# Kernel optimization log

Measured on AMD Instinct MI355X. Metric: run time of the kernel, lower is better.

The kernel has to match this reference:

```python
import jax, jax.numpy as jnp
import numpy as np

N_NODES = 50000
N_EDGES = 1600000
HIDDEN = 128
N_RBF = 50


def _linear_init(key, fan_in, fan_out):
    # mimic torch nn.Linear default init: U(-1/sqrt(fan_in), 1/sqrt(fan_in))
    kw, kb = jax.random.split(key)
    bound = 1.0 / np.sqrt(fan_in)
    W = jax.random.uniform(kw, (fan_in, fan_out), minval=-bound, maxval=bound, dtype=jnp.float32)
    b = jax.random.uniform(kb, (fan_out,), minval=-bound, maxval=bound, dtype=jnp.float32)
    return W, b


def setup_inputs() -> dict:
    key = jax.random.key(0)
    ks = jax.random.split(key, 9)
    x = jax.random.normal(ks[0], (N_NODES, HIDDEN), dtype=jnp.float32)
    edge_index = jax.random.randint(ks[1], (2, N_EDGES), 0, N_NODES, dtype=jnp.int32)
    edge_attr = jax.random.uniform(ks[2], (N_EDGES, N_RBF), dtype=jnp.float32)
    fW1, fb1 = _linear_init(ks[3], N_RBF, HIDDEN)
    fW2, fb2 = _linear_init(ks[4], HIDDEN, HIDDEN)
    dW, db = _linear_init(ks[5], HIDDEN, HIDDEN)
    uW1, ub1 = _linear_init(ks[6], HIDDEN, HIDDEN)
    uW2, ub2 = _linear_init(ks[7], HIDDEN, HIDDEN)
    return {
        "x": x, "edge_index": edge_index, "edge_attr": edge_attr,
        "fW1": fW1, "fb1": fb1, "fW2": fW2, "fb2": fb2,
        "dW": dW, "db": db,
        "uW1": uW1, "ub1": ub1, "uW2": uW2, "ub2": ub2,
    }


def reference(x, edge_index, edge_attr, fW1, fb1, fW2, fb2, dW, db, uW1, ub1, uW2, ub2):
    src, dst = edge_index[0], edge_index[1]
    # filter network: Linear -> SiLU -> Linear on edge RBF features [E, n_rbf] -> [E, H]
    filters = jax.nn.silu(edge_attr @ fW1 + fb1) @ fW2 + fb2
    # messages: dense(x[src]) * filters  [E, H]
    messages = (x[src] @ dW + db) * filters
    # scatter-add to destination nodes
    aggregated = jax.ops.segment_sum(messages, dst, num_segments=x.shape[0])
    # update MLP + residual
    upd = jax.nn.silu(aggregated @ uW1 + ub1) @ uW2 + ub2
    return x + upd
```

## Files before the change

### kernel.cpp

```cpp
#include <hip/hip_runtime.h>

#define H    128
#define RBF  50
#define K1   64
#define EB   64
#define NB   32
#define NBLK 1024

typedef _Float16 f16;
typedef _Float16 f16x4 __attribute__((ext_vector_type(4)));
typedef _Float16 f16x8 __attribute__((ext_vector_type(8)));
typedef float    f32x4 __attribute__((ext_vector_type(4)));

#define HS_LD 136

__device__ __forceinline__ float silu_f(float a) {
    return a / (1.0f + __expf(-a));
}


__global__ __launch_bounds__(256) void hist_kernel(
    const int* __restrict__ dst, int* __restrict__ counts, int E)
{
    for (int i = blockIdx.x * 256 + threadIdx.x; i < E; i += gridDim.x * 256)
        atomicAdd(&counts[dst[i]], 1);
}

__global__ __launch_bounds__(256) void scan1_kernel(
    const int* __restrict__ counts, int* __restrict__ ofs, int* __restrict__ bsum, int N)
{
    __shared__ int s[256];
    const int t = threadIdx.x;
    const int g = blockIdx.x * 256 + t;
    int v = (g < N) ? counts[g] : 0;
    s[t] = v; __syncthreads();
    for (int off = 1; off < 256; off <<= 1) {
        int u = 0; if (t >= off) u = s[t - off];
        __syncthreads(); s[t] += u; __syncthreads();
    }
    if (g < N) ofs[g] = s[t] - v;
    if (t == 255) bsum[blockIdx.x] = s[255];
}
__global__ __launch_bounds__(256) void scan2_kernel(int* __restrict__ bsum, int nb)
{
    __shared__ int s[256];
    const int t = threadIdx.x;
    int v = (t < nb) ? bsum[t] : 0;
    s[t] = v; __syncthreads();
    for (int off = 1; off < 256; off <<= 1) {
        int u = 0; if (t >= off) u = s[t - off];
        __syncthreads(); s[t] += u; __syncthreads();
    }
    if (t < nb) bsum[t] = s[t] - v;
}
__global__ __launch_bounds__(256) void scan3_kernel(
    int* __restrict__ ofs, int* __restrict__ cursor, const int* __restrict__ bsum, int N)
{
    int g = blockIdx.x * 256 + threadIdx.x;
    if (g < N) {
        int v = ofs[g] + bsum[blockIdx.x];
        ofs[g] = v;
        cursor[g] = v;
    }
}

__global__ __launch_bounds__(256) void ranges_kernel(
    const int* __restrict__ ofs, int* __restrict__ nstart, int* __restrict__ estart,
    int N, int E, int B)
{
    int b = blockIdx.x * 256 + threadIdx.x;
    if (b > B) return;
    if (b == B) { nstart[B] = N; estart[B] = E; return; }
    long long cb = (long long)b * E / B;
    int lo = 0, hi = N;
    while (lo < hi) {
        int mid = (lo + hi) >> 1;
        int val = (mid < N) ? ofs[mid] : E;
        if (val < (int)cb) lo = mid + 1; else hi = mid;
    }
    nstart[b] = lo;
    estart[b] = (lo < N) ? ofs[lo] : E;
}

__global__ __launch_bounds__(256) void scatter_kernel(
    const int* __restrict__ src, const int* __restrict__ dst,
    int* __restrict__ cursor, int* __restrict__ rank, int2* __restrict__ sd, int E)
{
    for (int i = blockIdx.x * 256 + threadIdx.x; i < E; i += gridDim.x * 256) {
        int d = dst[i];
        int pos = atomicAdd(&cursor[d], 1);
        rank[i] = pos;
        sd[pos] = make_int2(src[i], d);
    }
}

__global__ __launch_bounds__(256) void permute_ea_kernel(
    const float* __restrict__ ea, const int* __restrict__ rank,
    f16* __restrict__ ea16, int E)
{
    const int tid = threadIdx.x;
    const int e = blockIdx.x * EB + (tid >> 2);
    const int s = tid & 3;
    if (e >= E) return;
    const int p = rank[e];
    const float* rp = ea + (size_t)e * RBF;

    const float4 a = *(const float4*)(rp + s * 8);
    const float4 b = *(const float4*)(rp + s * 8 + 4);
    float4 c4 = {}, d4 = {};
    if (s < 2) {
        c4 = *(const float4*)(rp + 32 + s * 8);
        d4 = *(const float4*)(rp + 36 + s * 8);
    } else if (s == 2) {
        const float2 t2 = *(const float2*)(rp + 48);
        c4.x = t2.x; c4.y = t2.y;
    }
    f16x8 v1, v2;
    v1[0]=(f16)a.x; v1[1]=(f16)a.y; v1[2]=(f16)a.z; v1[3]=(f16)a.w;
    v1[4]=(f16)b.x; v1[5]=(f16)b.y; v1[6]=(f16)b.z; v1[7]=(f16)b.w;
    v2[0]=(f16)c4.x; v2[1]=(f16)c4.y; v2[2]=(f16)c4.z; v2[3]=(f16)c4.w;
    v2[4]=(f16)d4.x; v2[5]=(f16)d4.y; v2[6]=(f16)d4.z; v2[7]=(f16)d4.w;

    f16* op = ea16 + (size_t)p * K1;
    *(f16x8*)(op + s * 8)      = v1;
    *(f16x8*)(op + 32 + s * 8) = v2;
}


__global__ __launch_bounds__(256) void convert_weights_kernel(
    const float* __restrict__ fW1, const float* __restrict__ fW2,
    f16* __restrict__ Wt1, f16* __restrict__ Wt2)
{
    int i = blockIdx.x * 256 + threadIdx.x;
    if (i < H * K1) {
        int n = i >> 6, k = i & (K1 - 1);
        Wt1[i] = (k < RBF) ? (f16)fW1[k * H + n] : (f16)0.f;
    }
    int j = i - H * K1;
    if (j >= 0 && j < H * H) {
        int n = j >> 7, k = j & (H - 1);
        Wt2[j] = (f16)fW2[k * H + n];
    }
}

__global__ __launch_bounds__(256) void compute_h_kernel(
    const float* __restrict__ x, const float* __restrict__ dW,
    const float* __restrict__ db, f16* __restrict__ h, int N)
{
    __shared__ float xs[NB][H];
    const int tid = threadIdx.x;
    const int n0  = blockIdx.x * NB;
    for (int idx = tid; idx < NB * H; idx += 256) {
        int r = idx >> 7, c = idx & (H - 1);
        int n = n0 + r;
        xs[r][c] = (n < N) ? x[(size_t)n * H + c] : 0.f;
    }
    __syncthreads();
    const int j  = tid & (H - 1);
    const int rb = (tid >> 7) * 16;
    float acc[16];
    const float b = db[j];
#pragma unroll
    for (int r = 0; r < 16; ++r) acc[r] = b;
    for (int kq = 0; kq < H / 4; ++kq) {
        const int k = kq * 4;
        const float w0 = dW[(k + 0) * H + j];
        const float w1 = dW[(k + 1) * H + j];
        const float w2 = dW[(k + 2) * H + j];
        const float w3 = dW[(k + 3) * H + j];
#pragma unroll
        for (int r = 0; r < 16; ++r) {
            const float4 v = *(const float4*)&xs[rb + r][k];
            acc[r] = fmaf(v.x, w0, fmaf(v.y, w1, fmaf(v.z, w2, fmaf(v.w, w3, acc[r]))));
        }
    }
#pragma unroll
    for (int r = 0; r < 16; ++r) {
        int n = n0 + rb + r;
        if (n < N) h[(size_t)n * H + j] = (f16)acc[r];
    }
}

__global__ __launch_bounds__(256, 4) void edge_fused_kernel(
    const f16* __restrict__ ea16, const int2* __restrict__ sd,
    const f16* __restrict__ Wt1, const f16* __restrict__ Wt2,
    const float* __restrict__ fb1, const float* __restrict__ fb2,
    const f16* __restrict__ h, float* __restrict__ out,
    const int* __restrict__ nstart, const int* __restrict__ estart, int E)
{
    __shared__ __align__(16) f16 uni[8192];
    __shared__ __align__(16) f16 h_s[EB * HS_LD];
    __shared__ int dst_s[EB];

    const int tid  = threadIdx.x;
    const int lane = tid & 63;
    const int wv   = tid >> 6;
    const int wr   = (wv >> 1) * 32;
    const int wc   = (wv & 1) * 64;
    const int fr   = lane & 15;
    const int qw   = lane >> 4;
    const int kb   = qw * 8;

    const int j = tid >> 2;
    const int s = tid & 3;

    f16x8 B1[4][2];
    f16x8 B2[4][4];
    float b1v[4], b2v[4];
#pragma unroll
    for (int ct = 0; ct < 4; ++ct) {
        const int col = wc + ct * 16 + fr;
#pragma unroll
        for (int ks = 0; ks < 2; ++ks)
            B1[ct][ks] = *(const f16x8*)&Wt1[col * K1 + ks * 32 + kb];
#pragma unroll
        for (int ks = 0; ks < 4; ++ks)
            B2[ct][ks] = *(const f16x8*)&Wt2[col * H + ks * 32 + kb];
        b1v[ct] = fb1[col];
        b2v[ct] = fb2[col];
    }

    const int ns = nstart[blockIdx.x], ne = nstart[blockIdx.x + 1];
    const int e0 = estart[blockIdx.x], e1 = estart[blockIdx.x + 1];

    if (e0 >= e1) {
        for (int idx = tid; idx < (ne - ns) * H; idx += 256)
            out[(size_t)ns * H + idx] = 0.f;
        return;
    }

    const int col128 = tid & 127;
    int   curdst = ns;
    float accv   = 0.f;

    int2 sdP;
    { int idx = e0 + j; idx = (idx < e1) ? idx : (e1 - 1); sdP = sd[idx]; }

    for (int tb = e0; tb < e1; tb += EB) {
        int2 sdN;
        { int idx = tb + EB + j; idx = (idx < e1) ? idx : (e1 - 1); sdN = sd[idx]; }

        {
            const f16* hp = h + (size_t)sdP.x * H + s * 8;
            const f16x8 h0 = *(const f16x8*)(hp);
            const f16x8 h1 = *(const f16x8*)(hp + 32);
            const f16x8 h2 = *(const f16x8*)(hp + 64);
            const f16x8 h3 = *(const f16x8*)(hp + 96);

            const int pe = tb + j;
            const f16* ep = ea16 + (size_t)((pe < E) ? pe : (E - 1)) * K1;
            const f16x8 ev1 = *(const f16x8*)(ep + s * 8);
            const f16x8 ev2 = *(const f16x8*)(ep + 32 + s * 8);

            *(f16x8*)&h_s[j * HS_LD +  0 + s * 8] = h0;
            *(f16x8*)&h_s[j * HS_LD + 32 + s * 8] = h1;
            *(f16x8*)&h_s[j * HS_LD + 64 + s * 8] = h2;
            *(f16x8*)&h_s[j * HS_LD + 96 + s * 8] = h3;
            *(f16x8*)((char*)uni + (size_t)(((s)     * 64 + j) * 16)) = ev1;
            *(f16x8*)((char*)uni + (size_t)(((4 + s) * 64 + j) * 16)) = ev2;
            if (s == 0) dst_s[j] = (pe < e1) ? sdP.y : ne;
        }
        __syncthreads();

        f32x4 acc1[2][4];
#pragma unroll
        for (int rt = 0; rt < 2; ++rt)
#pragma unroll
            for (int ct = 0; ct < 4; ++ct)
                acc1[rt][ct] = (f32x4){b1v[ct], b1v[ct], b1v[ct], b1v[ct]};
#pragma unroll
        for (int ks = 0; ks < 2; ++ks) {
            const f16x8 A0 = *(const f16x8*)((char*)uni + (size_t)(((ks * 4 + qw) * 64 + wr + fr) * 16));
            const f16x8 A1 = *(const f16x8*)((char*)uni + (size_t)(((ks * 4 + qw) * 64 + wr + 16 + fr) * 16));
#pragma unroll
            for (int ct = 0; ct < 4; ++ct) {
                acc1[0][ct] = __builtin_amdgcn_mfma_f32_16x16x32_f16(A0, B1[ct][ks], acc1[0][ct], 0, 0, 0);
                acc1[1][ct] = __builtin_amdgcn_mfma_f32_16x16x32_f16(A1, B1[ct][ks], acc1[1][ct], 0, 0, 0);
            }
        }
        __syncthreads();

#pragma unroll
        for (int rt = 0; rt < 2; ++rt)
#pragma unroll
            for (int ct = 0; ct < 4; ++ct)
#pragma unroll
                for (int m = 0; m < 4; ++m) {
                    const int er = wr + rt * 16 + qw * 4 + m;
                    const int c  = wc + ct * 16 + fr;
                    *(f16*)((char*)uni + (size_t)(((c >> 3) * 64 + er) * 16 + (c & 7) * 2)) =
                        (f16)silu_f(acc1[rt][ct][m]);
                }
        __syncthreads();

        f32x4 acc2[2][4];
#pragma unroll
        for (int rt = 0; rt < 2; ++rt)
#pragma unroll
            for (int ct = 0; ct < 4; ++ct)
                acc2[rt][ct] = (f32x4){b2v[ct], b2v[ct], b2v[ct], b2v[ct]};
#pragma unroll
        for (int ks = 0; ks < 4; ++ks) {
            const f16x8 A0 = *(const f16x8*)((char*)uni + (size_t)(((ks * 4 + qw) * 64 + wr + fr) * 16));
            const f16x8 A1 = *(const f16x8*)((char*)uni + (size_t)(((ks * 4 + qw) * 64 + wr + 16 + fr) * 16));
#pragma unroll
            for (int ct = 0; ct < 4; ++ct) {
                acc2[0][ct] = __builtin_amdgcn_mfma_f32_16x16x32_f16(A0, B2[ct][ks], acc2[0][ct], 0, 0, 0);
                acc2[1][ct] = __builtin_amdgcn_mfma_f32_16x16x32_f16(A1, B2[ct][ks], acc2[1][ct], 0, 0, 0);
            }
        }

#pragma unroll
        for (int rt = 0; rt < 2; ++rt)
#pragma unroll
            for (int ct = 0; ct < 4; ++ct)
#pragma unroll
                for (int m = 0; m < 4; ++m) {
                    const int er = wr + rt * 16 + qw * 4 + m;
                    const int c  = wc + ct * 16 + fr;
                    f16* p = &h_s[er * HS_LD + c];
                    *p = (f16)((float)*p * acc2[rt][ct][m]);
                }
        __syncthreads();

        if (tid < 128) {
            for (int r = 0; r < EB; ++r) {
                const int d = dst_s[r];
                const float v = (float)h_s[r * HS_LD + col128];
                if (d != curdst) {
                    out[(size_t)curdst * H + col128] = accv;
                    for (int n = curdst + 1; n < d; ++n) out[(size_t)n * H + col128] = 0.f;
                    curdst = d; accv = 0.f;
                }
                if (d < ne) accv += v;
            }
        }
        __syncthreads();

        sdP = sdN;
    }

    if (tid < 128 && curdst < ne) {
        out[(size_t)curdst * H + col128] = accv;
        for (int n = curdst + 1; n < ne; ++n) out[(size_t)n * H + col128] = 0.f;
    }
}

__global__ __launch_bounds__(256) void update_kernel(
    const float* __restrict__ x,
    const float* __restrict__ uW1, const float* __restrict__ ub1,
    const float* __restrict__ uW2, const float* __restrict__ ub2,
    float* __restrict__ out, int N)
{
    __shared__ float as[NB][H];
    __shared__ float ts[NB][H];
    const int tid = threadIdx.x;
    const int n0  = blockIdx.x * NB;
    for (int idx = tid; idx < NB * H; idx += 256) {
        int r = idx >> 7, c = idx & (H - 1);
        int n = n0 + r;
        as[r][c] = (n < N) ? out[(size_t)n * H + c] : 0.f;
    }
    __syncthreads();
    const int j  = tid & (H - 1);
    const int rb = (tid >> 7) * 16;
    float acc[16];
    {
        const float b1 = ub1[j];
#pragma unroll
        for (int r = 0; r < 16; ++r) acc[r] = b1;
    }
    for (int kq = 0; kq < H / 4; ++kq) {
        const int k = kq * 4;
        const float w0 = uW1[(k + 0) * H + j];
        const float w1 = uW1[(k + 1) * H + j];
        const float w2 = uW1[(k + 2) * H + j];
        const float w3 = uW1[(k + 3) * H + j];
#pragma unroll
        for (int r = 0; r < 16; ++r) {
            const float4 v = *(const float4*)&as[rb + r][k];
            acc[r] = fmaf(v.x, w0, fmaf(v.y, w1, fmaf(v.z, w2, fmaf(v.w, w3, acc[r]))));
        }
    }
#pragma unroll
    for (int r = 0; r < 16; ++r) ts[rb + r][j] = silu_f(acc[r]);
    __syncthreads();
    {
        const float b2 = ub2[j];
#pragma unroll
        for (int r = 0; r < 16; ++r) acc[r] = b2;
    }
    for (int kq = 0; kq < H / 4; ++kq) {
        const int k = kq * 4;
        const float w0 = uW2[(k + 0) * H + j];
        const float w1 = uW2[(k + 1) * H + j];
        const float w2 = uW2[(k + 2) * H + j];
        const float w3 = uW2[(k + 3) * H + j];
#pragma unroll
        for (int r = 0; r < 16; ++r) {
            const float4 v = *(const float4*)&ts[rb + r][k];
            acc[r] = fmaf(v.x, w0, fmaf(v.y, w1, fmaf(v.z, w2, fmaf(v.w, w3, acc[r]))));
        }
    }
#pragma unroll
    for (int r = 0; r < 16; ++r) {
        int n = n0 + rb + r;
        if (n < N) out[(size_t)n * H + j] = x[(size_t)n * H + j] + acc[r];
    }
}

extern "C" void kernel_launch(void* const* d_in, const int* in_sizes, int n_in,
                              void* d_out, int out_size, void* d_ws, size_t ws_size,
                              hipStream_t stream) {
    const float* x   = (const float*)d_in[0];
    const int*   ei  = (const int*)  d_in[1];
    const float* ea  = (const float*)d_in[2];
    const float* fW1 = (const float*)d_in[3];
    const float* fb1 = (const float*)d_in[4];
    const float* fW2 = (const float*)d_in[5];
    const float* fb2 = (const float*)d_in[6];
    const float* dW  = (const float*)d_in[7];
    const float* db  = (const float*)d_in[8];
    const float* uW1 = (const float*)d_in[9];
    const float* ub1 = (const float*)d_in[10];
    const float* uW2 = (const float*)d_in[11];
    const float* ub2 = (const float*)d_in[12];

    float* out = (float*)d_out;
    const int N = in_sizes[0] / H;
    const int E = in_sizes[1] / 2;
    const int* src = ei;
    const int* dst = ei + E;

    char* ws = (char*)d_ws;
    size_t off = 0;
    auto alloc = [&](size_t bytes) { void* p = ws + off; off = (off + bytes + 255) & ~(size_t)255; return p; };
    f16*  h      = (f16*) alloc((size_t)N * H * sizeof(f16));
    f16*  Wt1    = (f16*) alloc((size_t)H * K1 * sizeof(f16));
    f16*  Wt2    = (f16*) alloc((size_t)H * H * sizeof(f16));
    int*  counts = (int*) alloc((size_t)N * sizeof(int));
    int*  ofs    = (int*) alloc((size_t)N * sizeof(int));
    int*  cursor = (int*) alloc((size_t)N * sizeof(int));
    int*  bsum   = (int*) alloc(256 * sizeof(int));
    int*  nstart = (int*) alloc((size_t)(NBLK + 1) * sizeof(int));
    int*  estart = (int*) alloc((size_t)(NBLK + 1) * sizeof(int));
    int*  rank   = (int*) alloc((size_t)E * sizeof(int));
    int2* sd     = (int2*)alloc((size_t)E * sizeof(int2));
    f16*  ea16   = (f16*) alloc((size_t)E * K1 * sizeof(f16));

    const int nscan  = (N + 255) / 256;
    const int ntiles = (E + EB - 1) / EB;

    hipMemsetAsync(counts, 0, (size_t)N * sizeof(int), stream);
    convert_weights_kernel<<<(H * K1 + H * H + 255) / 256, 256, 0, stream>>>(fW1, fW2, Wt1, Wt2);
    compute_h_kernel<<<(N + NB - 1) / NB, 256, 0, stream>>>(x, dW, db, h, N);

    hist_kernel<<<2048, 256, 0, stream>>>(dst, counts, E);
    scan1_kernel<<<nscan, 256, 0, stream>>>(counts, ofs, bsum, N);
    scan2_kernel<<<1, 256, 0, stream>>>(bsum, nscan);
    scan3_kernel<<<nscan, 256, 0, stream>>>(ofs, cursor, bsum, N);

    ranges_kernel<<<(NBLK + 256) / 256, 256, 0, stream>>>(ofs, nstart, estart, N, E, NBLK);
    scatter_kernel<<<2048, 256, 0, stream>>>(src, dst, cursor, rank, sd, E);
    permute_ea_kernel<<<ntiles, 256, 0, stream>>>(ea, rank, ea16, E);

    edge_fused_kernel<<<NBLK, 256, 0, stream>>>(
        ea16, sd, Wt1, Wt2, fb1, fb2, h, out, nstart, estart, E);

    update_kernel<<<(N + NB - 1) / NB, 256, 0, stream>>>(
        x, uW1, ub1, uW2, ub2, out, N);
}
```

Before: 947.3 us.

## Fuse prep kernels, merge scatter with edge-attr permute, double-buffer src/dst in LDS

Merges the weight conversion, node dense projection and destination histogram into one launch split by block index. Fuses the scatter and fp16 edge-attribute permutation into one pass, which drops the rank array and its extra read/write. In the edge kernel, src/dst indices are now staged through double-buffered shared memory, loaded by otherwise idle threads during the reduction phase, and gathered h rows are copied with a different lane mapping. The new build kernel has each thread write a full 128-byte row with weaker coalescing on the uncoalesced ea reads, which may offset the saved pass.

```diff
diff --git a/kernel.cpp b/kernel.cpp
--- a/kernel.cpp
+++ b/kernel.cpp
@@ -19,12 +19,67 @@
 }
 
 
-__global__ __launch_bounds__(256) void hist_kernel(
+__global__ __launch_bounds__(256) void prep1_kernel(
+    const float* __restrict__ x, const float* __restrict__ dW,
+    const float* __restrict__ db, f16* __restrict__ h, int N, int nH,
+    const float* __restrict__ fW1, const float* __restrict__ fW2,
+    f16* __restrict__ Wt1, f16* __restrict__ Wt2,
     const int* __restrict__ dst, int* __restrict__ counts, int E)
 {
-    for (int i = blockIdx.x * 256 + threadIdx.x; i < E; i += gridDim.x * 256)
-        atomicAdd(&counts[dst[i]], 1);
-}
+    __shared__ float xs[NB][H];
+    const int tid = threadIdx.x;
+    const int b   = blockIdx.x;
+
+    if (b < nH) {
+        const int n0 = b * NB;
+        for (int idx = tid; idx < NB * H; idx += 256) {
+            int r = idx >> 7, c = idx & (H - 1);
+            int n = n0 + r;
+            xs[r][c] = (n < N) ? x[(size_t)n * H + c] : 0.f;
+        }
+        __syncthreads();
+        const int j  = tid & (H - 1);
+        const int rb = (tid >> 7) * 16;
+        float acc[16];
+        const float bb = db[j];
+#pragma unroll
+        for (int r = 0; r < 16; ++r) acc[r] = bb;
+        for (int kq = 0; kq < H / 4; ++kq) {
+            const int k = kq * 4;
+            const float w0 = dW[(k + 0) * H + j];
+            const float w1 = dW[(k + 1) * H + j];
+            const float w2 = dW[(k + 2) * H + j];
+            const float w3 = dW[(k + 3) * H + j];
+#pragma unroll
+            for (int r = 0; r < 16; ++r) {
+                const float4 v = *(const float4*)&xs[rb + r][k];
+                acc[r] = fmaf(v.x, w0, fmaf(v.y, w1, fmaf(v.z, w2, fmaf(v.w, w3, acc[r]))));
+            }
+        }
+#pragma unroll
+        for (int r = 0; r < 16; ++r) {
+            int n = n0 + rb + r;
+            if (n < N) h[(size_t)n * H + j] = (f16)acc[r];
+        }
+    } else if (b < nH + 96) {
+        int i = (b - nH) * 256 + tid;
+        if (i < H * K1) {
+            int n = i >> 6, k = i & (K1 - 1);
+            Wt1[i] = (k < RBF) ? (f16)fW1[k * H + n] : (f16)0.f;
+        }
+        int jj = i - H * K1;
+        if (jj >= 0 && jj < H * H) {
+            int n = jj >> 7, k = jj & (H - 1);
+            Wt2[jj] = (f16)fW2[k * H + n];
+        }
+    } else {
+        const int hb  = b - nH - 96;
+        const int hgd = gridDim.x - nH - 96;
+        for (int i = hb * 256 + tid; i < E; i += hgd * 256)
+            atomicAdd(&counts[dst[i]], 1);
+    }
+}
+
 
 __global__ __launch_bounds__(256) void scan1_kernel(
     const int* __restrict__ counts, int* __restrict__ ofs, int* __restrict__ bsum, int N)
@@ -82,102 +137,36 @@
     estart[b] = (lo < N) ? ofs[lo] : E;
 }
 
-__global__ __launch_bounds__(256) void scatter_kernel(
-    const int* __restrict__ src, const int* __restrict__ dst,
-    int* __restrict__ cursor, int* __restrict__ rank, int2* __restrict__ sd, int E)
-{
-    for (int i = blockIdx.x * 256 + threadIdx.x; i < E; i += gridDim.x * 256) {
-        int d = dst[i];
-        int pos = atomicAdd(&cursor[d], 1);
-        rank[i] = pos;
-        sd[pos] = make_int2(src[i], d);
-    }
-}
-
-__global__ __launch_bounds__(256) void permute_ea_kernel(
-    const float* __restrict__ ea, const int* __restrict__ rank,
-    f16* __restrict__ ea16, int E)
-{
-    const int tid = threadIdx.x;
-    const int e = blockIdx.x * EB + (tid >> 2);
-    const int s = tid & 3;
-    if (e >= E) return;
-    const int p = rank[e];
-    const float* rp = ea + (size_t)e * RBF;
-
-    const float4 a = *(const float4*)(rp + s * 8);
-    const float4 b = *(const float4*)(rp + s * 8 + 4);
-    float4 c4 = {}, d4 = {};
-    if (s < 2) {
-        c4 = *(const float4*)(rp + 32 + s * 8);
-        d4 = *(const float4*)(rp + 36 + s * 8);
-    } else if (s == 2) {
-        const float2 t2 = *(const float2*)(rp + 48);
-        c4.x = t2.x; c4.y = t2.y;
-    }
-    f16x8 v1, v2;
-    v1[0]=(f16)a.x; v1[1]=(f16)a.y; v1[2]=(f16)a.z; v1[3]=(f16)a.w;
-    v1[4]=(f16)b.x; v1[5]=(f16)b.y; v1[6]=(f16)b.z; v1[7]=(f16)b.w;
-    v2[0]=(f16)c4.x; v2[1]=(f16)c4.y; v2[2]=(f16)c4.z; v2[3]=(f16)c4.w;
-    v2[4]=(f16)d4.x; v2[5]=(f16)d4.y; v2[6]=(f16)d4.z; v2[7]=(f16)d4.w;
-
-    f16* op = ea16 + (size_t)p * K1;
-    *(f16x8*)(op + s * 8)      = v1;
-    *(f16x8*)(op + 32 + s * 8) = v2;
-}
-
-
-__global__ __launch_bounds__(256) void convert_weights_kernel(
-    const float* __restrict__ fW1, const float* __restrict__ fW2,
-    f16* __restrict__ Wt1, f16* __restrict__ Wt2)
-{
-    int i = blockIdx.x * 256 + threadIdx.x;
-    if (i < H * K1) {
-        int n = i >> 6, k = i & (K1 - 1);
-        Wt1[i] = (k < RBF) ? (f16)fW1[k * H + n] : (f16)0.f;
-    }
-    int j = i - H * K1;
-    if (j >= 0 && j < H * H) {
-        int n = j >> 7, k = j & (H - 1);
-        Wt2[j] = (f16)fW2[k * H + n];
-    }
-}
-
-__global__ __launch_bounds__(256) void compute_h_kernel(
-    const float* __restrict__ x, const float* __restrict__ dW,
-    const float* __restrict__ db, f16* __restrict__ h, int N)
-{
-    __shared__ float xs[NB][H];
-    const int tid = threadIdx.x;
-    const int n0  = blockIdx.x * NB;
-    for (int idx = tid; idx < NB * H; idx += 256) {
-        int r = idx >> 7, c = idx & (H - 1);
-        int n = n0 + r;
-        xs[r][c] = (n < N) ? x[(size_t)n * H + c] : 0.f;
-    }
-    __syncthreads();
-    const int j  = tid & (H - 1);
-    const int rb = (tid >> 7) * 16;
-    float acc[16];
-    const float b = db[j];
-#pragma unroll
-    for (int r = 0; r < 16; ++r) acc[r] = b;
-    for (int kq = 0; kq < H / 4; ++kq) {
-        const int k = kq * 4;
-        const float w0 = dW[(k + 0) * H + j];
-        const float w1 = dW[(k + 1) * H + j];
-        const float w2 = dW[(k + 2) * H + j];
-        const float w3 = dW[(k + 3) * H + j];
-#pragma unroll
-        for (int r = 0; r < 16; ++r) {
-            const float4 v = *(const float4*)&xs[rb + r][k];
-            acc[r] = fmaf(v.x, w0, fmaf(v.y, w1, fmaf(v.z, w2, fmaf(v.w, w3, acc[r]))));
-        }
-    }
-#pragma unroll
-    for (int r = 0; r < 16; ++r) {
-        int n = n0 + rb + r;
-        if (n < N) h[(size_t)n * H + j] = (f16)acc[r];
+__global__ __launch_bounds__(256) void build_kernel(
+    const float* __restrict__ ea, const int* __restrict__ src, const int* __restrict__ dst,
+    int* __restrict__ cursor, int2* __restrict__ sd, f16* __restrict__ ea16, int E)
+{
+    for (int e = blockIdx.x * 256 + threadIdx.x; e < E; e += gridDim.x * 256) {
+        const int d = dst[e];
+        const int pos = atomicAdd(&cursor[d], 1);
+        sd[pos] = make_int2(src[e], d);
+
+        const float* rp = ea + (size_t)e * RBF;
+        f16* op = ea16 + (size_t)pos * K1;
+        f16x8 v[8];
+#pragma unroll
+        for (int q = 0; q < 6; ++q) {
+            const float4 a = *(const float4*)(rp + q * 8);
+            const float4 b = *(const float4*)(rp + q * 8 + 4);
+            f16x8 t;
+            t[0]=(f16)a.x; t[1]=(f16)a.y; t[2]=(f16)a.z; t[3]=(f16)a.w;
+            t[4]=(f16)b.x; t[5]=(f16)b.y; t[6]=(f16)b.z; t[7]=(f16)b.w;
+            v[q] = t;
+        }
+        {
+            const float2 a = *(const float2*)(rp + 48);
+            f16x8 t = {};
+            t[0]=(f16)a.x; t[1]=(f16)a.y;
+            v[6] = t;
+        }
+        v[7] = (f16x8){};
+#pragma unroll
+        for (int q = 0; q < 8; ++q) *(f16x8*)(op + q * 8) = v[q];
     }
 }
 
@@ -186,11 +175,12 @@
     const f16* __restrict__ Wt1, const f16* __restrict__ Wt2,
     const float* __restrict__ fb1, const float* __restrict__ fb2,
     const f16* __restrict__ h, float* __restrict__ out,
-    const int* __restrict__ nstart, const int* __restrict__ estart, int E)
+    const int* __restrict__ nstart, const int* __restrict__ estart)
 {
     __shared__ __align__(16) f16 uni[8192];
     __shared__ __align__(16) f16 h_s[EB * HS_LD];
-    __shared__ int dst_s[EB];
+    __shared__ int src_s[2][EB];
+    __shared__ int dst_s[2][EB];
 
     const int tid  = threadIdx.x;
     const int lane = tid & 63;
@@ -232,33 +222,34 @@
     const int col128 = tid & 127;
     int   curdst = ns;
     float accv   = 0.f;
-
-    int2 sdP;
-    { int idx = e0 + j; idx = (idx < e1) ? idx : (e1 - 1); sdP = sd[idx]; }
+    int   cur    = 0;
+
+    if (tid < EB) {
+        int idx = e0 + tid; idx = (idx < e1) ? idx : (e1 - 1);
+        int2 v = sd[idx];
+        src_s[0][tid] = v.x;
+        dst_s[0][tid] = (e0 + tid < e1) ? v.y : ne;
+    }
+    __syncthreads();
 
     for (int tb = e0; tb < e1; tb += EB) {
-        int2 sdN;
-        { int idx = tb + EB + j; idx = (idx < e1) ? idx : (e1 - 1); sdN = sd[idx]; }
-
         {
-            const f16* hp = h + (size_t)sdP.x * H + s * 8;
-            const f16x8 h0 = *(const f16x8*)(hp);
-            const f16x8 h1 = *(const f16x8*)(hp + 32);
-            const f16x8 h2 = *(const f16x8*)(hp + 64);
-            const f16x8 h3 = *(const f16x8*)(hp + 96);
-
+#pragma unroll
+            for (int i = 0; i < 2; ++i) {
+                const int row = (tid >> 3) + i * 32;
+                const int ch  = tid & 7;
+                const f16* hp = h + (size_t)src_s[cur][row] * H;
+#pragma unroll
+                for (int half = 0; half < 2; ++half)
+                    *(f16x8*)&h_s[row * HS_LD + half * 64 + ch * 8] =
+                        *(const f16x8*)(hp + half * 64 + ch * 8);
+            }
             const int pe = tb + j;
-            const f16* ep = ea16 + (size_t)((pe < E) ? pe : (E - 1)) * K1;
+            const f16* ep = ea16 + (size_t)((pe < e1) ? pe : (e1 - 1)) * K1;
             const f16x8 ev1 = *(const f16x8*)(ep + s * 8);
             const f16x8 ev2 = *(const f16x8*)(ep + 32 + s * 8);
-
-            *(f16x8*)&h_s[j * HS_LD +  0 + s * 8] = h0;
-            *(f16x8*)&h_s[j * HS_LD + 32 + s * 8] = h1;
-            *(f16x8*)&h_s[j * HS_LD + 64 + s * 8] = h2;
-            *(f16x8*)&h_s[j * HS_LD + 96 + s * 8] = h3;
             *(f16x8*)((char*)uni + (size_t)(((s)     * 64 + j) * 16)) = ev1;
             *(f16x8*)((char*)uni + (size_t)(((4 + s) * 64 + j) * 16)) = ev2;
-            if (s == 0) dst_s[j] = (pe < e1) ? sdP.y : ne;
         }
         __syncthreads();
 
@@ -324,8 +315,9 @@
         __syncthreads();
 
         if (tid < 128) {
+            const int* ds = dst_s[cur];
             for (int r = 0; r < EB; ++r) {
-                const int d = dst_s[r];
+                const int d = ds[r];
                 const float v = (float)h_s[r * HS_LD + col128];
                 if (d != curdst) {
                     out[(size_t)curdst * H + col128] = accv;
@@ -334,10 +326,16 @@
                 }
                 if (d < ne) accv += v;
             }
-        }
-        __syncthreads();
-
-        sdP = sdN;
+        } else if (tid < 128 + EB) {
+            const int r = tid - 128;
+            int idx = tb + EB + r; idx = (idx < e1) ? idx : (e1 - 1);
+            int2 v = sd[idx];
+            src_s[cur ^ 1][r] = v.x;
+            dst_s[cur ^ 1][r] = (tb + EB + r < e1) ? v.y : ne;
+        }
+        __syncthreads();
+
+        cur ^= 1;
     }
 
     if (tid < 128 && curdst < ne) {
@@ -444,29 +442,28 @@
     int*  bsum   = (int*) alloc(256 * sizeof(int));
     int*  nstart = (int*) alloc((size_t)(NBLK + 1) * sizeof(int));
     int*  estart = (int*) alloc((size_t)(NBLK + 1) * sizeof(int));
-    int*  rank   = (int*) alloc((size_t)E * sizeof(int));
     int2* sd     = (int2*)alloc((size_t)E * sizeof(int2));
     f16*  ea16   = (f16*) alloc((size_t)E * K1 * sizeof(f16));
 
-    const int nscan  = (N + 255) / 256;
-    const int ntiles = (E + EB - 1) / EB;
+    const int nH    = (N + NB - 1) / NB;
+    const int nscan = (N + 255) / 256;
 
     hipMemsetAsync(counts, 0, (size_t)N * sizeof(int), stream);
-    convert_weights_kernel<<<(H * K1 + H * H + 255) / 256, 256, 0, stream>>>(fW1, fW2, Wt1, Wt2);
-    compute_h_kernel<<<(N + NB - 1) / NB, 256, 0, stream>>>(x, dW, db, h, N);
-
-    hist_kernel<<<2048, 256, 0, stream>>>(dst, counts, E);
+
+    prep1_kernel<<<nH + 96 + 2048, 256, 0, stream>>>(
+        x, dW, db, h, N, nH, fW1, fW2, Wt1, Wt2, dst, counts, E);
+
     scan1_kernel<<<nscan, 256, 0, stream>>>(counts, ofs, bsum, N);
     scan2_kernel<<<1, 256, 0, stream>>>(bsum, nscan);
     scan3_kernel<<<nscan, 256, 0, stream>>>(ofs, cursor, bsum, N);
 
     ranges_kernel<<<(NBLK + 256) / 256, 256, 0, stream>>>(ofs, nstart, estart, N, E, NBLK);
-    scatter_kernel<<<2048, 256, 0, stream>>>(src, dst, cursor, rank, sd, E);
-    permute_ea_kernel<<<ntiles, 256, 0, stream>>>(ea, rank, ea16, E);
+
+    build_kernel<<<2048, 256, 0, stream>>>(ea, src, dst, cursor, sd, ea16, E);
 
     edge_fused_kernel<<<NBLK, 256, 0, stream>>>(
-        ea16, sd, Wt1, Wt2, fb1, fb2, h, out, nstart, estart, E);
-
-    update_kernel<<<(N + NB - 1) / NB, 256, 0, stream>>>(
+        ea16, sd, Wt1, Wt2, fb1, fb2, h, out, nstart, estart);
+
+    update_kernel<<<nH, 256, 0, stream>>>(
         x, uW1, ub1, uW2, ub2, out, N);
 }
```

Result: faster. 894.1 us (-5.6%).
